# Kernel tuning notes

Measured on AMD Instinct MI355X. Metric: run time of the kernel, lower is better.

Reference implementation:

```python
import jax, jax.numpy as jnp
import numpy as np

N_NODES = 8192
N_EDGES = 65536
IN_DIM = 768
HIDDEN = 4096
N_CLASSES = 16


def setup_inputs() -> dict:
    key = jax.random.key(0)
    k1, k2, k3, k4 = jax.random.split(key, 4)
    x = jax.random.normal(k1, (N_NODES, IN_DIM), dtype=jnp.float32)
    edge_index = jax.random.randint(k2, (2, N_EDGES), 0, N_NODES, dtype=jnp.int64)
    # Glorot-ish init scale
    W1 = jax.random.normal(k3, (IN_DIM, HIDDEN), dtype=jnp.float32) * (1.0 / np.sqrt(IN_DIM))
    b1 = jnp.zeros((HIDDEN,), dtype=jnp.float32)
    W2 = jax.random.normal(k4, (HIDDEN, N_CLASSES), dtype=jnp.float32) * (1.0 / np.sqrt(HIDDEN))
    b2 = jnp.zeros((N_CLASSES,), dtype=jnp.float32)
    return {"x": x, "edge_index": edge_index, "W1": W1, "b1": b1, "W2": W2, "b2": b2}


def reference(x, edge_index, W1, b1, W2, b2):
    # GCNConv (PyG defaults): add self-loops, symmetric deg^-1/2 normalization,
    # transform-then-aggregate, plus bias. Then ReLU -> (dropout=identity at
    # inference) -> Linear -> log_softmax.
    N = x.shape[0]
    loops = jnp.arange(N, dtype=edge_index.dtype)
    src = jnp.concatenate([edge_index[0], loops])  # [E+N]
    dst = jnp.concatenate([edge_index[1], loops])  # [E+N]

    h = x @ W1  # [N, HIDDEN] dense GEMM

    deg = jax.ops.segment_sum(jnp.ones_like(dst, dtype=h.dtype), dst, num_segments=N)
    dinv = jnp.where(deg > 0, jax.lax.rsqrt(jnp.maximum(deg, 1e-12)), 0.0)
    norm = dinv[src] * dinv[dst]  # [E+N]

    agg = jax.ops.segment_sum(h[src] * norm[:, None], dst, num_segments=N)  # [N, HIDDEN]
    h = jax.nn.relu(agg + b1)

    logits = h @ W2 + b2  # [N, N_CLASSES]
    return jax.nn.log_softmax(logits, axis=1)
```

## Files before the change

kernel.cpp:

```cpp
#include <hip/hip_runtime.h>

#define N_NODES   8192
#define N_EDGES   65536
#define IN_DIM    768
#define HIDDEN    4096
#define N_CLASSES 16
#define SLOTS     64

typedef unsigned short ushort_t;
typedef __attribute__((ext_vector_type(8))) short bf16x8;
typedef __attribute__((ext_vector_type(4))) float f32x4;

__device__ __forceinline__ ushort_t f2bf(float f) {
    union { float f; unsigned i; } v; v.f = f;
    unsigned r = v.i + 0x7FFFu + ((v.i >> 16) & 1u);
    return (ushort_t)(r >> 16);
}
__device__ __forceinline__ float bf2f(ushort_t u) {
    union { unsigned i; float f; } v; v.i = ((unsigned)u) << 16; return v.f;
}

#define GLD_LDS16(gp, lp) \
    __builtin_amdgcn_global_load_lds((const __attribute__((address_space(1))) void*)(gp), \
                                     (__attribute__((address_space(3))) void*)(lp), 16, 0, 0)

__device__ __forceinline__ int esrc(const int* ei, int f32mode, int e) {
    return f32mode ? ei[e] : ei[2 * e];
}
__device__ __forceinline__ int edst(const int* ei, int f32mode, int e) {
    return f32mode ? ei[N_EDGES + e] : ei[2 * N_EDGES + 2 * e];
}

__global__ __launch_bounds__(256) void conv_x(const float* __restrict__ x,
                                              ushort_t* __restrict__ xbf) {
    long i = (long)blockIdx.x * 1024 + threadIdx.x;
    #pragma unroll
    for (int p = 0; p < 4; p++) {
        float4 v = ((const float4*)x)[i + p * 256];
        ushort4 r = { f2bf(v.x), f2bf(v.y), f2bf(v.z), f2bf(v.w) };
        ((ushort4*)xbf)[i + p * 256] = r;
    }
}

__global__ __launch_bounds__(256) void conv_w1(const float* __restrict__ W1,
                                               ushort_t* __restrict__ W1T) {
    __shared__ ushort_t tile[32][33];
    int bb = blockIdx.x;
    int n0 = (bb & 127) * 32, k0 = (bb >> 7) * 32;
    int tx = threadIdx.x & 31, ty = threadIdx.x >> 5;
    #pragma unroll
    for (int j = 0; j < 4; j++) {
        int k = ty * 4 + j;
        tile[k][tx] = f2bf(W1[(k0 + k) * HIDDEN + n0 + tx]);
    }
    __syncthreads();
    #pragma unroll
    for (int j = 0; j < 4; j++) {
        int n = ty * 4 + j;
        W1T[(n0 + n) * IN_DIM + k0 + tx] = tile[tx][n];
    }
}

__global__ __launch_bounds__(256) void conv_w2(const float* __restrict__ W2,
                                               ushort_t* __restrict__ W2T) {
    __shared__ ushort_t ld[16 * 257];
    int t = threadIdx.x;
    int k0 = blockIdx.x * 256;
    const float4* src = (const float4*)(W2 + (long)(k0 + t) * N_CLASSES);
    #pragma unroll
    for (int j = 0; j < 4; j++) {
        float4 v = src[j];
        ld[(j * 4 + 0) * 257 + t] = f2bf(v.x);
        ld[(j * 4 + 1) * 257 + t] = f2bf(v.y);
        ld[(j * 4 + 2) * 257 + t] = f2bf(v.z);
        ld[(j * 4 + 3) * 257 + t] = f2bf(v.w);
    }
    __syncthreads();
    #pragma unroll
    for (int c = 0; c < 16; c++)
        W2T[c * HIDDEN + k0 + t] = ld[c * 257 + t];
}

__global__ __launch_bounds__(256) void bucket(const int* __restrict__ ei,
                                              int* __restrict__ cnt,
                                              int* __restrict__ slots,
                                              int* __restrict__ flag) {
    int b = blockIdx.x, t = threadIdx.x;
    __shared__ int sv[256];
    int v = 0;
    for (int e = t; e < 4096; e += 256) v |= ei[2 * e + 1];
    sv[t] = v;
    __syncthreads();
    for (int off = 128; off > 0; off >>= 1) {
        if (t < off) sv[t] |= sv[t + off];
        __syncthreads();
    }
    int f = (sv[0] != 0) ? 1 : 0;
    if (b == 0 && t == 0) *flag = f;
    int e = b * 256 + t;
    int s = esrc(ei, f, e), d = edst(ei, f, e);
    int p = atomicAdd(&cnt[d], 1);
    if (p < SLOTS) slots[d * SLOTS + p] = s;
}

__global__ __launch_bounds__(192) void aggregate(const ushort_t* __restrict__ xbf,
                                                 const int* __restrict__ cnt,
                                                 const int* __restrict__ slots,
                                                 const int* __restrict__ ei,
                                                 const int* __restrict__ flag,
                                                 ushort_t* __restrict__ xagg) {
    int w = threadIdx.x >> 6, l = threadIdx.x & 63;
    int d = blockIdx.x;
    int fo = w * 256 + l * 4;
    int cd = cnt[d];
    float wd = rsqrtf((float)(cd + 1));
    ushort4 sv = *(const ushort4*)(xbf + (long)d * IN_DIM + fo);
    float a0 = wd * bf2f(sv.x), a1 = wd * bf2f(sv.y);
    float a2 = wd * bf2f(sv.z), a3 = wd * bf2f(sv.w);

    if (cd <= SLOTS) {
        const int* sl = slots + d * SLOTS;
        int j = 0;
        for (; j + 4 <= cd; j += 4) {
            int s0 = sl[j], s1 = sl[j + 1], s2 = sl[j + 2], s3 = sl[j + 3];
            float w0 = rsqrtf((float)(cnt[s0] + 1));
            float w1 = rsqrtf((float)(cnt[s1] + 1));
            float w2 = rsqrtf((float)(cnt[s2] + 1));
            float w3 = rsqrtf((float)(cnt[s3] + 1));
            ushort4 v0 = *(const ushort4*)(xbf + (long)s0 * IN_DIM + fo);
            ushort4 v1 = *(const ushort4*)(xbf + (long)s1 * IN_DIM + fo);
            ushort4 v2 = *(const ushort4*)(xbf + (long)s2 * IN_DIM + fo);
            ushort4 v3 = *(const ushort4*)(xbf + (long)s3 * IN_DIM + fo);
            a0 = fmaf(w0, bf2f(v0.x), a0); a1 = fmaf(w0, bf2f(v0.y), a1);
            a2 = fmaf(w0, bf2f(v0.z), a2); a3 = fmaf(w0, bf2f(v0.w), a3);
            a0 = fmaf(w1, bf2f(v1.x), a0); a1 = fmaf(w1, bf2f(v1.y), a1);
            a2 = fmaf(w1, bf2f(v1.z), a2); a3 = fmaf(w1, bf2f(v1.w), a3);
            a0 = fmaf(w2, bf2f(v2.x), a0); a1 = fmaf(w2, bf2f(v2.y), a1);
            a2 = fmaf(w2, bf2f(v2.z), a2); a3 = fmaf(w2, bf2f(v2.w), a3);
            a0 = fmaf(w3, bf2f(v3.x), a0); a1 = fmaf(w3, bf2f(v3.y), a1);
            a2 = fmaf(w3, bf2f(v3.z), a2); a3 = fmaf(w3, bf2f(v3.w), a3);
        }
        for (; j < cd; j++) {
            int s = sl[j];
            float ws = rsqrtf((float)(cnt[s] + 1));
            ushort4 v = *(const ushort4*)(xbf + (long)s * IN_DIM + fo);
            a0 = fmaf(ws, bf2f(v.x), a0); a1 = fmaf(ws, bf2f(v.y), a1);
            a2 = fmaf(ws, bf2f(v.z), a2); a3 = fmaf(ws, bf2f(v.w), a3);
        }
    } else {
        int f = *flag;
        for (int e = 0; e < N_EDGES; e++) {
            if (edst(ei, f, e) == d) {
                int s = esrc(ei, f, e);
                float ws = rsqrtf((float)(cnt[s] + 1));
                ushort4 v = *(const ushort4*)(xbf + (long)s * IN_DIM + fo);
                a0 = fmaf(ws, bf2f(v.x), a0); a1 = fmaf(ws, bf2f(v.y), a1);
                a2 = fmaf(ws, bf2f(v.z), a2); a3 = fmaf(ws, bf2f(v.w), a3);
            }
        }
    }
    ushort4 r = { f2bf(a0 * wd), f2bf(a1 * wd), f2bf(a2 * wd), f2bf(a3 * wd) };
    *(ushort4*)(xagg + (long)d * IN_DIM + fo) = r;
}

__global__ __launch_bounds__(256) void gemm1_fused(const ushort_t* __restrict__ A,
                                                   const ushort_t* __restrict__ Bt,
                                                   const float* __restrict__ b1,
                                                   const ushort_t* __restrict__ W2T,
                                                   float* __restrict__ part) {
    __shared__ char smem[40960];
    ushort_t* ldsA = (ushort_t*)smem;
    ushort_t* ldsB = (ushort_t*)(smem + 16384);
    int bx = blockIdx.x & 31;
    int by = blockIdx.x >> 5;
    int m0 = by * 128, n0 = bx * 128;
    int t = threadIdx.x;
    int w = t >> 6, l = t & 63;
    int wm = w & 1, wn = w >> 1;
    int q = l >> 4, lm = l & 15;

    f32x4 acc[4][4] = {};

    const ushort_t* Ag = A + (long)m0 * IN_DIM;
    const ushort_t* Bg = Bt + (long)n0 * IN_DIM;

    int offA[4], offB[4];
    #pragma unroll
    for (int mt = 0; mt < 4; mt++) {
        int m = wm * 64 + mt * 16 + lm;
        offA[mt] = m * 32 + (q ^ ((m >> 1) & 3)) * 8;
    }
    #pragma unroll
    for (int nt = 0; nt < 4; nt++) {
        int n = wn * 64 + nt * 16 + lm;
        offB[nt] = n * 32 + (q ^ ((n >> 1) & 3)) * 8;
    }

    int srow[2], scg[2];
    #pragma unroll
    for (int i = 0; i < 2; i++) {
        int L = i * 256 + t;
        srow[i] = L >> 2;
        scg[i] = (L & 3) ^ ((srow[i] >> 1) & 3);
    }

    for (int ks = 0; ks < IN_DIM; ks += 64) {
        __syncthreads();
        #pragma unroll
        for (int i = 0; i < 2; i++) {
            GLD_LDS16(Ag + srow[i] * IN_DIM + ks + scg[i] * 8, ldsA + (i * 256 + w * 64) * 8);
            GLD_LDS16(Bg + srow[i] * IN_DIM + ks + scg[i] * 8, ldsB + (i * 256 + w * 64) * 8);
        }
        #pragma unroll
        for (int i = 0; i < 2; i++) {
            GLD_LDS16(Ag + srow[i] * IN_DIM + (ks + 32) + scg[i] * 8, ldsA + 4096 + (i * 256 + w * 64) * 8);
            GLD_LDS16(Bg + srow[i] * IN_DIM + (ks + 32) + scg[i] * 8, ldsB + 4096 + (i * 256 + w * 64) * 8);
        }
        __syncthreads();

        #pragma unroll
        for (int j = 0; j < 2; j++) {
            bf16x8 af[4], bfr[4];
            #pragma unroll
            for (int mt = 0; mt < 4; mt++)
                af[mt] = *(const bf16x8*)(ldsA + j * 4096 + offA[mt]);
            #pragma unroll
            for (int nt = 0; nt < 4; nt++)
                bfr[nt] = *(const bf16x8*)(ldsB + j * 4096 + offB[nt]);
            #pragma unroll
            for (int mt = 0; mt < 4; mt++)
                #pragma unroll
                for (int nt = 0; nt < 4; nt++)
                    acc[mt][nt] = __builtin_amdgcn_mfma_f32_16x16x32_bf16(af[mt], bfr[nt], acc[mt][nt], 0, 0, 0);
        }
    }

    __syncthreads();
    const int RP = 80;
    ushort_t* myhl = (ushort_t*)smem + w * 64 * RP;

    float bias[4];
    #pragma unroll
    for (int nt = 0; nt < 4; nt++) bias[nt] = b1[n0 + wn * 64 + nt * 16 + lm];

    #pragma unroll
    for (int mt = 0; mt < 4; mt++) {
        #pragma unroll
        for (int nt = 0; nt < 4; nt++) {
            #pragma unroll
            for (int r = 0; r < 4; r++) {
                float v = acc[mt][nt][r] + bias[nt];
                v = v > 0.0f ? v : 0.0f;
                myhl[(mt * 16 + q * 4 + r) * RP + nt * 16 + lm] = f2bf(v);
            }
        }
    }

    f32x4 acc2[4] = {};
    #pragma unroll
    for (int kk = 0; kk < 2; kk++) {
        bf16x8 bf2 = *(const bf16x8*)(W2T + (long)lm * HIDDEN + n0 + wn * 64 + kk * 32 + q * 8);
        #pragma unroll
        for (int mt = 0; mt < 4; mt++) {
            bf16x8 a2 = *(const bf16x8*)(myhl + (mt * 16 + lm) * RP + kk * 32 + q * 8);
            acc2[mt] = __builtin_amdgcn_mfma_f32_16x16x32_bf16(a2, bf2, acc2[mt], 0, 0, 0);
        }
    }

    float* psum = (float*)smem;
    __syncthreads();
    if (wn == 1) {
        #pragma unroll
        for (int mt = 0; mt < 4; mt++)
            #pragma unroll
            for (int r = 0; r < 4; r++)
                psum[(wm * 64 + mt * 16 + q * 4 + r) * 17 + lm] = acc2[mt][r];
    }
    __syncthreads();
    if (wn == 0) {
        float* pslab = part + ((long)bx * N_NODES + m0 + wm * 64) * N_CLASSES;
        #pragma unroll
        for (int mt = 0; mt < 4; mt++)
            #pragma unroll
            for (int r = 0; r < 4; r++) {
                float v = acc2[mt][r] + psum[(wm * 64 + mt * 16 + q * 4 + r) * 17 + lm];
                pslab[(mt * 16 + q * 4 + r) * N_CLASSES + lm] = v;
            }
    }
}

__global__ __launch_bounds__(256) void reduce_softmax(const float* __restrict__ part,
                                                      const float* __restrict__ b2,
                                                      float* __restrict__ out) {
    int t = threadIdx.x;
    int row = blockIdx.x * 16 + (t >> 4);
    int cls = t & 15;
    float v = b2[cls];
    #pragma unroll
    for (int s = 0; s < 32; s++)
        v += part[((long)s * N_NODES + row) * N_CLASSES + cls];
    float mx = v;
    #pragma unroll
    for (int off = 1; off < 16; off <<= 1)
        mx = fmaxf(mx, __shfl_xor(mx, off, 64));
    float e = __expf(v - mx);
    float sm = e;
    #pragma unroll
    for (int off = 1; off < 16; off <<= 1)
        sm += __shfl_xor(sm, off, 64);
    out[(long)row * N_CLASSES + cls] = v - mx - __logf(sm);
}


extern "C" void kernel_launch(void* const* d_in, const int* in_sizes, int n_in,
                              void* d_out, int out_size, void* d_ws, size_t ws_size,
                              hipStream_t stream) {
    const float* x  = (const float*)d_in[0];
    const int*   ei = (const int*)d_in[1];
    const float* W1 = (const float*)d_in[2];
    const float* b1 = (const float*)d_in[3];
    const float* W2 = (const float*)d_in[4];
    const float* b2 = (const float*)d_in[5];
    float* out = (float*)d_out;
    char* ws = (char*)d_ws;

    float*    part  = (float*)(ws);
    ushort_t* xagg  = (ushort_t*)(ws + 16777216);
    ushort_t* xbf   = (ushort_t*)(ws + 29360128);
    ushort_t* W1T   = (ushort_t*)(ws + 41943040);
    ushort_t* W2T   = (ushort_t*)(ws + 48234496);
    int*      cnt   = (int*)(ws + 48365568);
    int*      slots = (int*)(ws + 48398336);
    int*      flag  = (int*)(ws + 50495488);

    hipMemsetAsync(cnt, 0, 32768, stream);
    conv_x<<<1536, 256, 0, stream>>>(x, xbf);
    bucket<<<256, 256, 0, stream>>>(ei, cnt, slots, flag);
    conv_w1<<<3072, 256, 0, stream>>>(W1, W1T);
    conv_w2<<<16, 256, 0, stream>>>(W2, W2T);
    aggregate<<<N_NODES, 192, 0, stream>>>(xbf, cnt, slots, ei, flag, xagg);
    gemm1_fused<<<(N_NODES / 128) * (HIDDEN / 128), 256, 0, stream>>>(xagg, W1T, b1, W2T, part);
    reduce_softmax<<<N_NODES / 16, 256, 0, stream>>>(part, b2, out);
}
```

Baseline: 184.6 us.

## Merge setup kernels into one launch and read GEMM A operand directly from global

The four preprocessing kernels (x conversion, W1 transpose, W2 transpose, edge bucketing) become one block-range-dispatched kernel, removing three launches and their serialization gaps. Separately, the main GEMM no longer stages the A tile through LDS. Each lane loads its A fragments straight from global memory, which halves LDS staging traffic but makes each wave re-read A rows from global/L2 without LDS reuse. The A loads are also no longer asynchronous global-to-LDS copies.

Result: slower. 230.5 us (+24.9%).

```diff
diff --git a/kernel.cpp b/kernel.cpp
--- a/kernel.cpp
+++ b/kernel.cpp
@@ -31,76 +31,74 @@
     return f32mode ? ei[N_EDGES + e] : ei[2 * N_EDGES + 2 * e];
 }
 
-__global__ __launch_bounds__(256) void conv_x(const float* __restrict__ x,
-                                              ushort_t* __restrict__ xbf) {
-    long i = (long)blockIdx.x * 1024 + threadIdx.x;
-    #pragma unroll
-    for (int p = 0; p < 4; p++) {
-        float4 v = ((const float4*)x)[i + p * 256];
-        ushort4 r = { f2bf(v.x), f2bf(v.y), f2bf(v.z), f2bf(v.w) };
-        ((ushort4*)xbf)[i + p * 256] = r;
-    }
-}
-
-__global__ __launch_bounds__(256) void conv_w1(const float* __restrict__ W1,
-                                               ushort_t* __restrict__ W1T) {
-    __shared__ ushort_t tile[32][33];
-    int bb = blockIdx.x;
-    int n0 = (bb & 127) * 32, k0 = (bb >> 7) * 32;
-    int tx = threadIdx.x & 31, ty = threadIdx.x >> 5;
-    #pragma unroll
-    for (int j = 0; j < 4; j++) {
-        int k = ty * 4 + j;
-        tile[k][tx] = f2bf(W1[(k0 + k) * HIDDEN + n0 + tx]);
-    }
-    __syncthreads();
-    #pragma unroll
-    for (int j = 0; j < 4; j++) {
-        int n = ty * 4 + j;
-        W1T[(n0 + n) * IN_DIM + k0 + tx] = tile[tx][n];
-    }
-}
-
-__global__ __launch_bounds__(256) void conv_w2(const float* __restrict__ W2,
-                                               ushort_t* __restrict__ W2T) {
-    __shared__ ushort_t ld[16 * 257];
-    int t = threadIdx.x;
-    int k0 = blockIdx.x * 256;
-    const float4* src = (const float4*)(W2 + (long)(k0 + t) * N_CLASSES);
-    #pragma unroll
-    for (int j = 0; j < 4; j++) {
-        float4 v = src[j];
-        ld[(j * 4 + 0) * 257 + t] = f2bf(v.x);
-        ld[(j * 4 + 1) * 257 + t] = f2bf(v.y);
-        ld[(j * 4 + 2) * 257 + t] = f2bf(v.z);
-        ld[(j * 4 + 3) * 257 + t] = f2bf(v.w);
-    }
-    __syncthreads();
-    #pragma unroll
-    for (int c = 0; c < 16; c++)
-        W2T[c * HIDDEN + k0 + t] = ld[c * 257 + t];
-}
-
-__global__ __launch_bounds__(256) void bucket(const int* __restrict__ ei,
-                                              int* __restrict__ cnt,
-                                              int* __restrict__ slots,
-                                              int* __restrict__ flag) {
+__global__ __launch_bounds__(256) void setup_all(const float* __restrict__ x,
+                                                 ushort_t* __restrict__ xbf,
+                                                 const float* __restrict__ W1,
+                                                 ushort_t* __restrict__ W1T,
+                                                 const float* __restrict__ W2,
+                                                 ushort_t* __restrict__ W2T,
+                                                 const int* __restrict__ ei,
+                                                 int* __restrict__ cnt,
+                                                 int* __restrict__ slots,
+                                                 int* __restrict__ flag) {
     int b = blockIdx.x, t = threadIdx.x;
-    __shared__ int sv[256];
-    int v = 0;
-    for (int e = t; e < 4096; e += 256) v |= ei[2 * e + 1];
-    sv[t] = v;
-    __syncthreads();
-    for (int off = 128; off > 0; off >>= 1) {
-        if (t < off) sv[t] |= sv[t + off];
-        __syncthreads();
-    }
-    int f = (sv[0] != 0) ? 1 : 0;
-    if (b == 0 && t == 0) *flag = f;
-    int e = b * 256 + t;
-    int s = esrc(ei, f, e), d = edst(ei, f, e);
-    int p = atomicAdd(&cnt[d], 1);
-    if (p < SLOTS) slots[d * SLOTS + p] = s;
+    if (b < 16) {
+        __shared__ ushort_t ld[16 * 257];
+        int k0 = b * 256;
+        const float4* src = (const float4*)(W2 + (long)(k0 + t) * N_CLASSES);
+        #pragma unroll
+        for (int j = 0; j < 4; j++) {
+            float4 v = src[j];
+            ld[(j * 4 + 0) * 257 + t] = f2bf(v.x);
+            ld[(j * 4 + 1) * 257 + t] = f2bf(v.y);
+            ld[(j * 4 + 2) * 257 + t] = f2bf(v.z);
+            ld[(j * 4 + 3) * 257 + t] = f2bf(v.w);
+        }
+        __syncthreads();
+        #pragma unroll
+        for (int c = 0; c < 16; c++)
+            W2T[c * HIDDEN + k0 + t] = ld[c * 257 + t];
+    } else if (b < 1552) {
+        long i = (long)(b - 16) * 1024 + t;
+        #pragma unroll
+        for (int p = 0; p < 4; p++) {
+            float4 v = ((const float4*)x)[i + p * 256];
+            ushort4 r = { f2bf(v.x), f2bf(v.y), f2bf(v.z), f2bf(v.w) };
+            ((ushort4*)xbf)[i + p * 256] = r;
+        }
+    } else if (b < 4624) {
+        __shared__ ushort_t tile[32][33];
+        int bb = b - 1552;
+        int n0 = (bb & 127) * 32, k0 = (bb >> 7) * 32;
+        int tx = t & 31, ty = t >> 5;
+        #pragma unroll
+        for (int j = 0; j < 4; j++) {
+            int k = ty * 4 + j;
+            tile[k][tx] = f2bf(W1[(k0 + k) * HIDDEN + n0 + tx]);
+        }
+        __syncthreads();
+        #pragma unroll
+        for (int j = 0; j < 4; j++) {
+            int n = ty * 4 + j;
+            W1T[(n0 + n) * IN_DIM + k0 + tx] = tile[tx][n];
+        }
+    } else {
+        __shared__ int sv[256];
+        int v = 0;
+        for (int e = t; e < 4096; e += 256) v |= ei[2 * e + 1];
+        sv[t] = v;
+        __syncthreads();
+        for (int off = 128; off > 0; off >>= 1) {
+            if (t < off) sv[t] |= sv[t + off];
+            __syncthreads();
+        }
+        int f = (sv[0] != 0) ? 1 : 0;
+        if (b == 4624 && t == 0) *flag = f;
+        int e = (b - 4624) * 256 + t;
+        int s = esrc(ei, f, e), d = edst(ei, f, e);
+        int p = atomicAdd(&cnt[d], 1);
+        if (p < SLOTS) slots[d * SLOTS + p] = s;
+    }
 }
 
 __global__ __launch_bounds__(192) void aggregate(const ushort_t* __restrict__ xbf,
@@ -169,8 +167,7 @@
                                                    const ushort_t* __restrict__ W2T,
                                                    float* __restrict__ part) {
     __shared__ char smem[40960];
-    ushort_t* ldsA = (ushort_t*)smem;
-    ushort_t* ldsB = (ushort_t*)(smem + 16384);
+    ushort_t* ldsB = (ushort_t*)smem;
     int bx = blockIdx.x & 31;
     int by = blockIdx.x >> 5;
     int m0 = by * 128, n0 = bx * 128;
@@ -181,15 +178,14 @@
 
     f32x4 acc[4][4] = {};
 
-    const ushort_t* Ag = A + (long)m0 * IN_DIM;
     const ushort_t* Bg = Bt + (long)n0 * IN_DIM;
 
-    int offA[4], offB[4];
-    #pragma unroll
-    for (int mt = 0; mt < 4; mt++) {
-        int m = wm * 64 + mt * 16 + lm;
-        offA[mt] = m * 32 + (q ^ ((m >> 1) & 3)) * 8;
-    }
+    const ushort_t* pA[4];
+    #pragma unroll
+    for (int mt = 0; mt < 4; mt++)
+        pA[mt] = A + (long)(m0 + wm * 64 + mt * 16 + lm) * IN_DIM + q * 8;
+
+    int offB[4];
     #pragma unroll
     for (int nt = 0; nt < 4; nt++) {
         int n = wn * 64 + nt * 16 + lm;
@@ -207,15 +203,11 @@
     for (int ks = 0; ks < IN_DIM; ks += 64) {
         __syncthreads();
         #pragma unroll
-        for (int i = 0; i < 2; i++) {
-            GLD_LDS16(Ag + srow[i] * IN_DIM + ks + scg[i] * 8, ldsA + (i * 256 + w * 64) * 8);
+        for (int i = 0; i < 2; i++)
             GLD_LDS16(Bg + srow[i] * IN_DIM + ks + scg[i] * 8, ldsB + (i * 256 + w * 64) * 8);
-        }
-        #pragma unroll
-        for (int i = 0; i < 2; i++) {
-            GLD_LDS16(Ag + srow[i] * IN_DIM + (ks + 32) + scg[i] * 8, ldsA + 4096 + (i * 256 + w * 64) * 8);
+        #pragma unroll
+        for (int i = 0; i < 2; i++)
             GLD_LDS16(Bg + srow[i] * IN_DIM + (ks + 32) + scg[i] * 8, ldsB + 4096 + (i * 256 + w * 64) * 8);
-        }
         __syncthreads();
 
         #pragma unroll
@@ -223,7 +215,7 @@
             bf16x8 af[4], bfr[4];
             #pragma unroll
             for (int mt = 0; mt < 4; mt++)
-                af[mt] = *(const bf16x8*)(ldsA + j * 4096 + offA[mt]);
+                af[mt] = *(const bf16x8*)(pA[mt] + ks + j * 32);
             #pragma unroll
             for (int nt = 0; nt < 4; nt++)
                 bfr[nt] = *(const bf16x8*)(ldsB + j * 4096 + offB[nt]);
@@ -334,10 +326,7 @@
     int*      flag  = (int*)(ws + 50495488);
 
     hipMemsetAsync(cnt, 0, 32768, stream);
-    conv_x<<<1536, 256, 0, stream>>>(x, xbf);
-    bucket<<<256, 256, 0, stream>>>(ei, cnt, slots, flag);
-    conv_w1<<<3072, 256, 0, stream>>>(W1, W1T);
-    conv_w2<<<16, 256, 0, stream>>>(W2, W2T);
+    setup_all<<<4880, 256, 0, stream>>>(x, xbf, W1, W1T, W2, W2T, ei, cnt, slots, flag);
     aggregate<<<N_NODES, 192, 0, stream>>>(xbf, cnt, slots, ei, flag, xagg);
     gemm1_fused<<<(N_NODES / 128) * (HIDDEN / 128), 256, 0, stream>>>(xagg, W1T, b1, W2T, part);
     reduce_softmax<<<N_NODES / 16, 256, 0, stream>>>(part, b2, out);
```
